# Performance work log

Hardware: AMD Instinct MI355X
Metric: run time of the kernel (lower is better)

## Reference

```python
import jax, jax.numpy as jnp
import numpy as np

DIM = 512


def layer_norm(x, w, b, eps=1e-5):
    mu = jnp.mean(x, axis=-1, keepdims=True)
    var = jnp.var(x, axis=-1, keepdims=True)
    return (x - mu) * jax.lax.rsqrt(var + eps) * w + b


def setup_inputs() -> dict:
    key = jax.random.key(0)
    kx, = jax.random.split(key, 1)
    x = jax.random.normal(kx, (8, 2048, DIM), dtype=jnp.float32)
    ln_w = jnp.ones((DIM,), dtype=jnp.float32)
    ln_b = jnp.zeros((DIM,), dtype=jnp.float32)
    q_diag = jnp.ones((DIM,), dtype=jnp.float32)
    k_diag = jnp.ones((DIM,), dtype=jnp.float32)
    v_diag = jnp.ones((DIM,), dtype=jnp.float32)
    return {"x": x, "ln_w": ln_w, "ln_b": ln_b,
            "q_diag": q_diag, "k_diag": k_diag, "v_diag": v_diag}


def reference(x, ln_w, ln_b, q_diag, k_diag, v_diag):
    # x: [B, N, D]
    xn = layer_norm(x, ln_w, ln_b)
    q = xn * q_diag
    k = xn * k_diag
    v = xn * v_diag
    scale = 1.0 / jnp.sqrt(jnp.float32(xn.shape[-1]))
    sim = jnp.einsum('bnd,bmd->bnm', q, k) * scale  # [B, N, N]
    attn = jax.nn.softmax(sim, axis=-1)
    atn_x = jnp.einsum('bnm,bmd->bnd', attn, v)
    # dropout is identity at inference (p=0)
    return xn + atn_x
```

## Files before the change

kernel.cpp:

```cpp
#include <hip/hip_runtime.h>
#include <hip/hip_bf16.h>
#include <stdint.h>
#include <math.h>

typedef __bf16 bf16_t;
typedef bf16_t bf16x8 __attribute__((ext_vector_type(8)));
typedef float f32x4 __attribute__((ext_vector_type(4)));

#define B_DIM 8
#define N_DIM 2048
#define D_DIM 512
#define QK_SCALE_L2E 0.063758716f
#define M_SHIFT2 5.7707801635558536f

#define KOFF 0
#define VOFF 98304
#define SMEM_ATTN 163840

__device__ __forceinline__ bf16_t f2bf(float f) {
    uint32_t u = __builtin_bit_cast(uint32_t, f);
    u += 0x7FFFu + ((u >> 16) & 1u);
    uint16_t h = (uint16_t)(u >> 16);
    return __builtin_bit_cast(bf16_t, h);
}

__device__ __forceinline__ float fexp2(float x) {
    float r;
    asm("v_exp_f32 %0, %1" : "=v"(r) : "v"(x));
    return r;
}

__global__ __launch_bounds__(512) void prep_fused(
    const float* __restrict__ x, const float* __restrict__ w, const float* __restrict__ bia,
    const float* __restrict__ qd, const float* __restrict__ kd, const float* __restrict__ vd,
    bf16_t* __restrict__ xnb, float* __restrict__ xnf,
    bf16_t* __restrict__ qb, bf16_t* __restrict__ kb, bf16_t* __restrict__ vT)
{
    extern __shared__ char pmem[];
    bf16_t (*vt)[512] = (bf16_t(*)[512])pmem;

    const int bid = blockIdx.x;
    const int b  = bid >> 5;
    const int n0 = (bid & 31) * 64;
    const int tid  = threadIdx.x;
    const int wid  = tid >> 6;
    const int lane = tid & 63;
    const int d    = lane * 8;

    float wv[8], bv[8], qv[8], kv[8], vv[8];
    {
        float4 t;
        t = *(const float4*)(w  + d);     wv[0]=t.x; wv[1]=t.y; wv[2]=t.z; wv[3]=t.w;
        t = *(const float4*)(w  + d + 4); wv[4]=t.x; wv[5]=t.y; wv[6]=t.z; wv[7]=t.w;
        t = *(const float4*)(bia+ d);     bv[0]=t.x; bv[1]=t.y; bv[2]=t.z; bv[3]=t.w;
        t = *(const float4*)(bia+ d + 4); bv[4]=t.x; bv[5]=t.y; bv[6]=t.z; bv[7]=t.w;
        t = *(const float4*)(qd + d);     qv[0]=t.x; qv[1]=t.y; qv[2]=t.z; qv[3]=t.w;
        t = *(const float4*)(qd + d + 4); qv[4]=t.x; qv[5]=t.y; qv[6]=t.z; qv[7]=t.w;
        t = *(const float4*)(kd + d);     kv[0]=t.x; kv[1]=t.y; kv[2]=t.z; kv[3]=t.w;
        t = *(const float4*)(kd + d + 4); kv[4]=t.x; kv[5]=t.y; kv[6]=t.z; kv[7]=t.w;
        t = *(const float4*)(vd + d);     vv[0]=t.x; vv[1]=t.y; vv[2]=t.z; vv[3]=t.w;
        t = *(const float4*)(vd + d + 4); vv[4]=t.x; vv[5]=t.y; vv[6]=t.z; vv[7]=t.w;
    }

    for (int r = 0; r < 8; r++) {
        int nl = wid*8 + r;
        size_t row  = (size_t)b*N_DIM + n0 + nl;
        size_t base = row*D_DIM + d;
        float xv[8];
        {
            float4 a0 = *(const float4*)(x + base);
            float4 a1 = *(const float4*)(x + base + 4);
            xv[0]=a0.x; xv[1]=a0.y; xv[2]=a0.z; xv[3]=a0.w;
            xv[4]=a1.x; xv[5]=a1.y; xv[6]=a1.z; xv[7]=a1.w;
        }
        float s = 0.f, s2 = 0.f;
        #pragma unroll
        for (int j = 0; j < 8; j++) { s += xv[j]; s2 += xv[j]*xv[j]; }
        #pragma unroll
        for (int m = 1; m < 64; m <<= 1) {
            s  += __shfl_xor(s,  m);
            s2 += __shfl_xor(s2, m);
        }
        float mu   = s  * (1.f/512.f);
        float var  = s2 * (1.f/512.f) - mu*mu;
        float rstd = rsqrtf(var + 1e-5f);

        float xo[8];
        bf16x8 qo, ko, xb, vb;
        #pragma unroll
        for (int j = 0; j < 8; j++) {
            float v = (xv[j] - mu) * rstd * wv[j] + bv[j];
            xo[j] = v;
            xb[j] = f2bf(v);
            qo[j] = f2bf(v * qv[j] * QK_SCALE_L2E);
            ko[j] = f2bf(v * kv[j]);
            vb[j] = f2bf(v * vv[j]);
        }
        if (xnb) {
            *(bf16x8*)(xnb + base) = xb;
        } else {
            float4 o0 = {xo[0],xo[1],xo[2],xo[3]};
            float4 o1 = {xo[4],xo[5],xo[6],xo[7]};
            *(float4*)(xnf + base)     = o0;
            *(float4*)(xnf + base + 4) = o1;
        }
        *(bf16x8*)(qb + base) = qo;
        *(bf16x8*)(kb + base) = ko;
        *(bf16x8*)(&vt[nl][d]) = vb;
    }
    __syncthreads();

    {
        const int dd = tid;
        const int salt = (dd >> 1) & 3;
        bf16_t* vrow = vT + ((size_t)(b*D_DIM + dd))*N_DIM + n0;
        #pragma unroll
        for (int kb2 = 0; kb2 < 2; kb2++) {
            #pragma unroll
            for (int sp = 0; sp < 4; sp++) {
                int gg = sp ^ salt;
                bf16x8 o;
                #pragma unroll
                for (int e = 0; e < 4; e++) o[e]   = vt[kb2*32 + 4*gg + e][dd];
                #pragma unroll
                for (int e = 0; e < 4; e++) o[4+e] = vt[kb2*32 + 16 + 4*gg + e][dd];
                *(bf16x8*)(vrow + kb2*32 + sp*8) = o;
            }
        }
    }
}

__global__ __launch_bounds__(512, 2) void attn9(
    const bf16_t* __restrict__ qb, const bf16_t* __restrict__ kb,
    const bf16_t* __restrict__ vT, bf16_t* __restrict__ opart, float* __restrict__ stats)
{
    extern __shared__ char smem[];

    const int bid = blockIdx.x;
    const int xcd = bid & 7, jj = bid >> 3;
    const int grp = xcd + 8*(jj >> 4);
    const int qt  = jj & 15;
    const int b   = grp >> 1;
    const int s   = grp & 1;
    const int q0  = qt * 128;
    const int n0base = s * 1024;

    const int tid  = threadIdx.x;
    const int wid  = tid >> 6;
    const int lane = tid & 63;
    const int g    = lane >> 4;
    const int li   = lane & 15;

    const bf16_t* kb_b = kb + (size_t)b * N_DIM * D_DIM;
    const bf16_t* vT_b = vT + (size_t)b * D_DIM * N_DIM;

    bf16x8 qf[16];
    {
        const bf16_t* qp = qb + ((size_t)(b*N_DIM + q0 + wid*16 + li)) * D_DIM + g*8;
        #pragma unroll
        for (int ks = 0; ks < 16; ks++)
            qf[ks] = *(const bf16x8*)(qp + ks*32);
    }

    f32x4 acc[32];
    const f32x4 zf = {0.f, 0.f, 0.f, 0.f};
    #pragma unroll
    for (int j = 0; j < 32; j++) acc[j] = zf;

    float l_r = 0.f;

    const int Lk = (lane ^ wid) * 8;
    auto stageK = [&](int slot, int t) {
        const int kstart = n0base + t*32;
        char* kdst = smem + KOFF + slot*32768;
        #pragma unroll
        for (int v = 0; v < 4; v++) {
            int row = v*8 + wid;
            const bf16_t* src = kb_b + (size_t)(kstart + row)*D_DIM + Lk;
            __builtin_amdgcn_global_load_lds((const void*)src, (void*)(kdst + row*1024), 16, 0, 0);
        }
    };
    auto stageV = [&](int buf, int t) {
        const int kstart = n0base + t*32;
        char* vdst = smem + VOFF + buf*32768 + wid*4096;
        const int drow = wid*64 + (lane >> 2);
        const bf16_t* src0 = vT_b + (size_t)drow*N_DIM + kstart + (lane & 3)*8;
        #pragma unroll
        for (int v = 0; v < 4; v++) {
            __builtin_amdgcn_global_load_lds((const void*)(src0 + (size_t)(v*16)*N_DIM),
                                             (void*)(vdst + v*1024), 16, 0, 0);
        }
    };

    stageK(0, 0);
    stageV(0, 0);
    stageK(1, 1);
    asm volatile("s_waitcnt vmcnt(4)" ::: "memory");
    __builtin_amdgcn_s_barrier();

    const int sw  = li & 7;
    const int vsw = (g ^ ((li >> 1) & 3)) << 4;

    int kc = 0;

    #pragma unroll 1
    for (int t = 0; t < 32; ++t) {
        const int vbuf = t & 1;
        const int ks2  = (kc + 2 >= 3) ? (kc + 2 - 3) : (kc + 2);

        if (t < 31) stageV(vbuf ^ 1, t + 1);
        if (t < 30) stageK(ks2, t + 2);
        __builtin_amdgcn_sched_barrier(0);

        const char* kr0 = smem + KOFF + kc*32768 + li*1024;
        const char* kr1 = kr0 + 16*1024;
        f32x4 s0 = zf, s1 = zf;
        __builtin_amdgcn_s_setprio(1);
        #pragma unroll
        for (int ks = 0; ks < 16; ks++) {
            int phys = (((ks << 2) + g) ^ sw) << 4;
            bf16x8 k0 = *(const bf16x8*)(kr0 + phys);
            bf16x8 k1 = *(const bf16x8*)(kr1 + phys);
            s0 = __builtin_amdgcn_mfma_f32_16x16x32_bf16(k0, qf[ks], s0, 0, 0, 0);
            s1 = __builtin_amdgcn_mfma_f32_16x16x32_bf16(k1, qf[ks], s1, 0, 0, 0);
        }
        __builtin_amdgcn_s_setprio(0);

        float p0[4], p1[4];
        #pragma unroll
        for (int r = 0; r < 4; r++) {
            p0[r] = fexp2(s0[r] - M_SHIFT2);
            p1[r] = fexp2(s1[r] - M_SHIFT2);
        }
        l_r += ((p0[0]+p0[1]) + (p0[2]+p0[3])) + ((p1[0]+p1[1]) + (p1[2]+p1[3]));
        bf16x8 af;
        af[0]=f2bf(p0[0]); af[1]=f2bf(p0[1]); af[2]=f2bf(p0[2]); af[3]=f2bf(p0[3]);
        af[4]=f2bf(p1[0]); af[5]=f2bf(p1[1]); af[6]=f2bf(p1[2]); af[7]=f2bf(p1[3]);

        const char* Vb = smem + VOFF + vbuf*32768 + li*64 + vsw;
        __builtin_amdgcn_s_setprio(1);
        #pragma unroll
        for (int j = 0; j < 32; j++) {
            bf16x8 bv = *(const bf16x8*)(Vb + j*1024);
            acc[j] = __builtin_amdgcn_mfma_f32_16x16x32_bf16(af, bv, acc[j], 0, 0, 0);
        }
        __builtin_amdgcn_s_setprio(0);

        if (t < 31) {
            if (t < 30) {
                asm volatile("s_waitcnt vmcnt(4) lgkmcnt(0)" ::: "memory");
            } else {
                asm volatile("s_waitcnt vmcnt(0) lgkmcnt(0)" ::: "memory");
            }
            __builtin_amdgcn_s_barrier();
        }

        kc = (kc + 1 >= 3) ? 0 : kc + 1;
    }

    l_r += __shfl_xor(l_r, 16);
    l_r += __shfl_xor(l_r, 32);

    bf16_t* op = opart + ((size_t)((s*8 + b)*N_DIM) + q0 + wid*16) * D_DIM;
    #pragma unroll
    for (int j = 0; j < 32; j++)
        #pragma unroll
        for (int r = 0; r < 4; r++)
            op[(size_t)(4*g + r)*D_DIM + j*16 + li] = f2bf(acc[j][r]);

    if (lane < 16) {
        stats[(size_t)(s*8 + b)*N_DIM + q0 + wid*16 + lane] = l_r;
    }
}

__global__ __launch_bounds__(256) void merge3(
    const bf16_t* __restrict__ opart, const float* __restrict__ stats,
    const bf16_t* __restrict__ xnb, float* __restrict__ out)
{
    int row  = (int)((blockIdx.x * blockDim.x + threadIdx.x) >> 6);
    int lane = threadIdx.x & 63;
    float l0 = stats[row];
    float l1 = stats[(size_t)16384 + row];
    float rden = 1.f / (l0 + l1);
    size_t base = (size_t)row * D_DIM + lane*8;
    bf16x8 a = *(const bf16x8*)(opart + base);
    bf16x8 c = *(const bf16x8*)(opart + (size_t)16384*D_DIM + base);
    float xv[8];
    if (xnb) {
        bf16x8 xb = *(const bf16x8*)(xnb + base);
        #pragma unroll
        for (int j = 0; j < 8; j++) xv[j] = (float)xb[j];
    } else {
        float4 x0 = *(const float4*)(out + base);
        float4 x1 = *(const float4*)(out + base + 4);
        xv[0]=x0.x; xv[1]=x0.y; xv[2]=x0.z; xv[3]=x0.w;
        xv[4]=x1.x; xv[5]=x1.y; xv[6]=x1.z; xv[7]=x1.w;
    }
    float o[8];
    #pragma unroll
    for (int j = 0; j < 8; j++) o[j] = xv[j] + ((float)a[j] + (float)c[j]) * rden;
    float4 r0 = {o[0], o[1], o[2], o[3]};
    float4 r1 = {o[4], o[5], o[6], o[7]};
    *(float4*)(out + base)     = r0;
    *(float4*)(out + base + 4) = r1;
}

extern "C" void kernel_launch(void* const* d_in, const int* in_sizes, int n_in,
                              void* d_out, int out_size, void* d_ws, size_t ws_size,
                              hipStream_t stream)
{
    const float* x  = (const float*)d_in[0];
    const float* lw = (const float*)d_in[1];
    const float* lb = (const float*)d_in[2];
    const float* qd = (const float*)d_in[3];
    const float* kd = (const float*)d_in[4];
    const float* vd = (const float*)d_in[5];
    float* out = (float*)d_out;

    const size_t MB = 1024u*1024u;
    char* ws = (char*)d_ws;
    bf16_t* qbuf  = (bf16_t*)(ws);
    bf16_t* kbuf  = (bf16_t*)(ws + 16*MB);
    bf16_t* vTb   = (bf16_t*)(ws + 32*MB);
    bf16_t* opart = (bf16_t*)(ws + 48*MB);
    float*  stats = (float*)(ws + 80*MB);
    bf16_t* xnb   = (ws_size >= 97*MB) ? (bf16_t*)(ws + 81*MB) : nullptr;

    hipFuncSetAttribute((const void*)prep_fused, hipFuncAttributeMaxDynamicSharedMemorySize, 65536);
    hipFuncSetAttribute((const void*)attn9, hipFuncAttributeMaxDynamicSharedMemorySize, SMEM_ATTN);

    prep_fused<<<256, 512, 65536, stream>>>(x, lw, lb, qd, kd, vd, xnb, out, qbuf, kbuf, vTb);
    attn9<<<256, 512, SMEM_ATTN, stream>>>(qbuf, kbuf, vTb, opart, stats);
    merge3<<<4096, 256, 0, stream>>>(opart, stats, xnb, out);
}
```

Before: 122.9 us.

## Switch attention to 32x32x16 MFMA with split-D waves and LDS score exchange

Rewrites the attention kernel to use 32x32x16 bf16 MFMA tiles: each pair of waves owns 32 query rows and splits the head dimension in halves. Each wave computes partial QK scores over its half, and the pair sums them through an LDS exchange guarded by an extra barrier. The V transpose layout in the prep kernel changes to match the new operand order. K is now double-buffered instead of triple-buffered. The aim is fewer MFMA instructions and fewer LDS reads per tile, at the cost of an extra barrier per iteration and a shallower prefetch pipeline.

```diff
diff --git a/kernel.cpp b/kernel.cpp
--- a/kernel.cpp
+++ b/kernel.cpp
@@ -6,6 +6,7 @@
 typedef __bf16 bf16_t;
 typedef bf16_t bf16x8 __attribute__((ext_vector_type(8)));
 typedef float f32x4 __attribute__((ext_vector_type(4)));
+typedef float f32x16 __attribute__((ext_vector_type(16)));
 
 #define B_DIM 8
 #define N_DIM 2048
@@ -14,7 +15,8 @@
 #define M_SHIFT2 5.7707801635558536f
 
 #define KOFF 0
-#define VOFF 98304
+#define VOFF 65536
+#define SXOFF 131072
 #define SMEM_ATTN 163840
 
 __device__ __forceinline__ bf16_t f2bf(float f) {
@@ -118,19 +120,20 @@
         for (int kb2 = 0; kb2 < 2; kb2++) {
             #pragma unroll
             for (int sp = 0; sp < 4; sp++) {
-                int gg = sp ^ salt;
+                int lam = sp ^ salt;
+                int kbase = (lam >> 1)*16 + (lam & 1)*4;
                 bf16x8 o;
                 #pragma unroll
-                for (int e = 0; e < 4; e++) o[e]   = vt[kb2*32 + 4*gg + e][dd];
+                for (int e = 0; e < 4; e++) o[e]   = vt[kb2*32 + kbase + e][dd];
                 #pragma unroll
-                for (int e = 0; e < 4; e++) o[4+e] = vt[kb2*32 + 16 + 4*gg + e][dd];
+                for (int e = 0; e < 4; e++) o[4+e] = vt[kb2*32 + kbase + 8 + e][dd];
                 *(bf16x8*)(vrow + kb2*32 + sp*8) = o;
             }
         }
     }
 }
 
-__global__ __launch_bounds__(512, 2) void attn9(
+__global__ __launch_bounds__(512, 2) void attn10(
     const bf16_t* __restrict__ qb, const bf16_t* __restrict__ kb,
     const bf16_t* __restrict__ vT, bf16_t* __restrict__ opart, float* __restrict__ stats)
 {
@@ -148,31 +151,34 @@
     const int tid  = threadIdx.x;
     const int wid  = tid >> 6;
     const int lane = tid & 63;
-    const int g    = lane >> 4;
-    const int li   = lane & 15;
+    const int qq   = wid >> 1;
+    const int dh   = wid & 1;
+    const int la   = lane & 31;
+    const int hi   = lane >> 5;
 
     const bf16_t* kb_b = kb + (size_t)b * N_DIM * D_DIM;
     const bf16_t* vT_b = vT + (size_t)b * D_DIM * N_DIM;
 
     bf16x8 qf[16];
     {
-        const bf16_t* qp = qb + ((size_t)(b*N_DIM + q0 + wid*16 + li)) * D_DIM + g*8;
+        const bf16_t* qp = qb + ((size_t)(b*N_DIM + q0 + qq*32 + la)) * D_DIM + dh*256 + hi*8;
         #pragma unroll
         for (int ks = 0; ks < 16; ks++)
-            qf[ks] = *(const bf16x8*)(qp + ks*32);
-    }
-
-    f32x4 acc[32];
-    const f32x4 zf = {0.f, 0.f, 0.f, 0.f};
+            qf[ks] = *(const bf16x8*)(qp + ks*16);
+    }
+
+    f32x16 acc[8];
     #pragma unroll
-    for (int j = 0; j < 32; j++) acc[j] = zf;
+    for (int dt = 0; dt < 8; dt++)
+        #pragma unroll
+        for (int e = 0; e < 16; e++) acc[dt][e] = 0.f;
 
     float l_r = 0.f;
 
     const int Lk = (lane ^ wid) * 8;
-    auto stageK = [&](int slot, int t) {
+    auto stageK = [&](int buf, int t) {
         const int kstart = n0base + t*32;
-        char* kdst = smem + KOFF + slot*32768;
+        char* kdst = smem + KOFF + buf*32768;
         #pragma unroll
         for (int v = 0; v < 4; v++) {
             int row = v*8 + wid;
@@ -194,82 +200,93 @@
 
     stageK(0, 0);
     stageV(0, 0);
-    stageK(1, 1);
-    asm volatile("s_waitcnt vmcnt(4)" ::: "memory");
+    asm volatile("s_waitcnt vmcnt(0)" ::: "memory");
     __builtin_amdgcn_s_barrier();
 
-    const int sw  = li & 7;
-    const int vsw = (g ^ ((li >> 1) & 3)) << 4;
-
-    int kc = 0;
+    const int ksalt  = la & 7;
+    const int vsalt  = (la >> 1) & 3;
+    const int sxsalt = lane & 3;
+    char* sxw = smem + SXOFF + wid*4096 + lane*64;
+    const char* sxr = smem + SXOFF + (wid^1)*4096 + lane*64;
 
     #pragma unroll 1
     for (int t = 0; t < 32; ++t) {
-        const int vbuf = t & 1;
-        const int ks2  = (kc + 2 >= 3) ? (kc + 2 - 3) : (kc + 2);
-
-        if (t < 31) stageV(vbuf ^ 1, t + 1);
-        if (t < 30) stageK(ks2, t + 2);
+        const int buf = t & 1;
+
+        if (t < 31) {
+            stageK(buf ^ 1, t + 1);
+            stageV(buf ^ 1, t + 1);
+        }
         __builtin_amdgcn_sched_barrier(0);
 
-        const char* kr0 = smem + KOFF + kc*32768 + li*1024;
-        const char* kr1 = kr0 + 16*1024;
-        f32x4 s0 = zf, s1 = zf;
+        const char* kr = smem + KOFF + buf*32768 + la*1024;
+        f32x16 Sp;
+        #pragma unroll
+        for (int e = 0; e < 16; e++) Sp[e] = 0.f;
         __builtin_amdgcn_s_setprio(1);
         #pragma unroll
         for (int ks = 0; ks < 16; ks++) {
-            int phys = (((ks << 2) + g) ^ sw) << 4;
-            bf16x8 k0 = *(const bf16x8*)(kr0 + phys);
-            bf16x8 k1 = *(const bf16x8*)(kr1 + phys);
-            s0 = __builtin_amdgcn_mfma_f32_16x16x32_bf16(k0, qf[ks], s0, 0, 0, 0);
-            s1 = __builtin_amdgcn_mfma_f32_16x16x32_bf16(k1, qf[ks], s1, 0, 0, 0);
+            int c = dh*32 + ks*2 + hi;
+            bf16x8 kf = *(const bf16x8*)(kr + ((c ^ ksalt) << 4));
+            Sp = __builtin_amdgcn_mfma_f32_32x32x16_bf16(kf, qf[ks], Sp, 0, 0, 0);
         }
         __builtin_amdgcn_s_setprio(0);
 
-        float p0[4], p1[4];
-        #pragma unroll
-        for (int r = 0; r < 4; r++) {
-            p0[r] = fexp2(s0[r] - M_SHIFT2);
-            p1[r] = fexp2(s1[r] - M_SHIFT2);
-        }
-        l_r += ((p0[0]+p0[1]) + (p0[2]+p0[3])) + ((p1[0]+p1[1]) + (p1[2]+p1[3]));
-        bf16x8 af;
-        af[0]=f2bf(p0[0]); af[1]=f2bf(p0[1]); af[2]=f2bf(p0[2]); af[3]=f2bf(p0[3]);
-        af[4]=f2bf(p1[0]); af[5]=f2bf(p1[1]); af[6]=f2bf(p1[2]); af[7]=f2bf(p1[3]);
-
-        const char* Vb = smem + VOFF + vbuf*32768 + li*64 + vsw;
+        #pragma unroll
+        for (int c2 = 0; c2 < 4; c2++) {
+            f32x4 wv4 = {Sp[c2*4+0], Sp[c2*4+1], Sp[c2*4+2], Sp[c2*4+3]};
+            *(f32x4*)(sxw + ((c2 ^ sxsalt) << 4)) = wv4;
+        }
+        asm volatile("s_waitcnt lgkmcnt(0)" ::: "memory");
+        __builtin_amdgcn_s_barrier();
+
+        float pv[16];
+        #pragma unroll
+        for (int c2 = 0; c2 < 4; c2++) {
+            f32x4 pr = *(const f32x4*)(sxr + ((c2 ^ sxsalt) << 4));
+            #pragma unroll
+            for (int e = 0; e < 4; e++)
+                pv[c2*4+e] = fexp2((Sp[c2*4+e] + pr[e]) - M_SHIFT2);
+        }
+        float ls = 0.f;
+        #pragma unroll
+        for (int r = 0; r < 16; r++) ls += pv[r];
+        l_r += ls;
+        bf16x8 af0, af1;
+        #pragma unroll
+        for (int j = 0; j < 8; j++) { af0[j] = f2bf(pv[j]); af1[j] = f2bf(pv[8+j]); }
+
+        const char* vr = smem + VOFF + buf*32768 + (size_t)(dh*256 + la)*64;
         __builtin_amdgcn_s_setprio(1);
         #pragma unroll
-        for (int j = 0; j < 32; j++) {
-            bf16x8 bv = *(const bf16x8*)(Vb + j*1024);
-            acc[j] = __builtin_amdgcn_mfma_f32_16x16x32_bf16(af, bv, acc[j], 0, 0, 0);
+        for (int dt = 0; dt < 8; dt++) {
+            const char* vrow = vr + dt*2048;
+            bf16x8 v0 = *(const bf16x8*)(vrow + (((0*2 + hi) ^ vsalt) << 4));
+            bf16x8 v1 = *(const bf16x8*)(vrow + (((1*2 + hi) ^ vsalt) << 4));
+            acc[dt] = __builtin_amdgcn_mfma_f32_32x32x16_bf16(af0, v0, acc[dt], 0, 0, 0);
+            acc[dt] = __builtin_amdgcn_mfma_f32_32x32x16_bf16(af1, v1, acc[dt], 0, 0, 0);
         }
         __builtin_amdgcn_s_setprio(0);
 
         if (t < 31) {
-            if (t < 30) {
-                asm volatile("s_waitcnt vmcnt(4) lgkmcnt(0)" ::: "memory");
-            } else {
-                asm volatile("s_waitcnt vmcnt(0) lgkmcnt(0)" ::: "memory");
-            }
+            asm volatile("s_waitcnt vmcnt(0) lgkmcnt(0)" ::: "memory");
             __builtin_amdgcn_s_barrier();
         }
-
-        kc = (kc + 1 >= 3) ? 0 : kc + 1;
-    }
-
-    l_r += __shfl_xor(l_r, 16);
+    }
+
     l_r += __shfl_xor(l_r, 32);
 
-    bf16_t* op = opart + ((size_t)((s*8 + b)*N_DIM) + q0 + wid*16) * D_DIM;
+    bf16_t* op = opart + ((size_t)((s*8 + b)*N_DIM) + q0 + qq*32) * D_DIM + dh*256;
     #pragma unroll
-    for (int j = 0; j < 32; j++)
-        #pragma unroll
-        for (int r = 0; r < 4; r++)
-            op[(size_t)(4*g + r)*D_DIM + j*16 + li] = f2bf(acc[j][r]);
-
-    if (lane < 16) {
-        stats[(size_t)(s*8 + b)*N_DIM + q0 + wid*16 + lane] = l_r;
+    for (int dt = 0; dt < 8; dt++)
+        #pragma unroll
+        for (int r = 0; r < 16; r++) {
+            int qrow = (r & 3) + 8*(r >> 2) + 4*hi;
+            op[(size_t)qrow*D_DIM + dt*32 + la] = f2bf(acc[dt][r]);
+        }
+
+    if (dh == 0 && lane < 32) {
+        stats[(size_t)(s*8 + b)*N_DIM + q0 + qq*32 + lane] = l_r;
     }
 }
 
@@ -327,9 +344,9 @@
     bf16_t* xnb   = (ws_size >= 97*MB) ? (bf16_t*)(ws + 81*MB) : nullptr;
 
     hipFuncSetAttribute((const void*)prep_fused, hipFuncAttributeMaxDynamicSharedMemorySize, 65536);
-    hipFuncSetAttribute((const void*)attn9, hipFuncAttributeMaxDynamicSharedMemorySize, SMEM_ATTN);
+    hipFuncSetAttribute((const void*)attn10, hipFuncAttributeMaxDynamicSharedMemorySize, SMEM_ATTN);
 
     prep_fused<<<256, 512, 65536, stream>>>(x, lw, lb, qd, kd, vd, xnb, out, qbuf, kbuf, vTb);
-    attn9<<<256, 512, SMEM_ATTN, stream>>>(qbuf, kbuf, vTb, opart, stats);
+    attn10<<<256, 512, SMEM_ATTN, stream>>>(qbuf, kbuf, vTb, opart, stats);
     merge3<<<4096, 256, 0, stream>>>(opart, stats, xnb, out);
 }
```

Result: slower. 152.3 us (+23.9%).
